# Kernel tuning notes

Measured on AMD Instinct MI355X. Metric: run time of the kernel, lower is better.

## Reference

```python
import jax, jax.numpy as jnp
import numpy as np

IMAGE_SIZE = 1024
DOWNSIZING = 64
THRESHOLD = 0.65  # default_threshold_target (threshold arg == 0)
NUM_BG_POINTS = 1
ORI_SHAPE = (2160, 3840)
EMBED_C, FEAT_H, FEAT_W = 256, 64, 64


def setup_inputs() -> dict:
    key = jax.random.key(0)
    k1, k2 = jax.random.split(key)
    image_embeddings = jax.random.normal(k1, (1, EMBED_C, FEAT_H, FEAT_W), dtype=jnp.float32)
    reference_feat = jax.random.normal(k2, (1, EMBED_C), dtype=jnp.float32) * 0.1
    ori_shape = jnp.array(ORI_SHAPE, dtype=jnp.int32)
    return {"image_embeddings": image_embeddings, "reference_feat": reference_feat, "ori_shape": ori_shape}


def _postprocess_masks(sim, H, W):
    # F.interpolate to (image_size, image_size), crop to pre-padded size, resize to ori_shape
    sim = jax.image.resize(sim, (1, 1, IMAGE_SIZE, IMAGE_SIZE), method="bilinear", antialias=False)
    scale = IMAGE_SIZE / max(H, W)
    ph = int(np.floor(H * scale + 0.5))
    pw = int(np.floor(W * scale + 0.5))
    sim = sim[..., :ph, :pw]
    return jax.image.resize(sim, (1, 1, H, W), method="bilinear", antialias=False)


def reference(image_embeddings, reference_feat, ori_shape):
    H, W = int(ori_shape[0]), int(ori_shape[1])
    # --- similarity map ---
    t = image_embeddings[0]                                   # (C, hf, wf)
    c, hf, wf = t.shape
    t = t / jnp.linalg.norm(t, axis=0, keepdims=True)         # channel-wise L2 norm
    sim = (reference_feat @ t.reshape(c, hf * wf)).reshape(1, 1, hf, wf)
    sim = _postprocess_masks(sim, H, W)
    m = sim[0, 0]                                             # (H, W)
    flat = m.reshape(-1)                                      # (H*W,)
    hw = H * W

    # --- background points: k smallest values ---
    _, bg_idx = jax.lax.top_k(-flat, NUM_BG_POINTS)
    bg_row = bg_idx // W
    bg_col = bg_idx % W
    bg_coords = jnp.stack([bg_col, bg_row], axis=1).astype(jnp.float32)  # (N, 2) = (x, y)

    # --- foreground points: grid-binned per-cell max (segment-max form of
    #     torch.where + unique + broadcast-equality + per-bin topk) ---
    ratio = IMAGE_SIZE / max(H, W)
    n_cells_side = IMAGE_SIZE // DOWNSIZING                    # 16; bounds grid rows/cols
    num_cells = n_cells_side * n_cells_side                    # 256 fixed
    idx = jnp.arange(hw, dtype=jnp.int32)
    ys = idx // W
    xs = idx % W
    gy = jnp.floor(ys * (ratio / DOWNSIZING)).astype(jnp.int32)
    gx = jnp.floor(xs * (ratio / DOWNSIZING)).astype(jnp.int32)
    seg = gy * n_cells_side + gx                               # grid id per pixel

    valid = flat > THRESHOLD
    masked = jnp.where(valid, flat, -jnp.inf)
    seg_max = jax.ops.segment_max(masked, seg, num_segments=num_cells)
    # first pixel achieving the cell max (matches torch.topk tie behavior)
    is_max = valid & (masked == seg_max[seg])
    cand = jnp.where(is_max, idx, hw)
    best = jax.ops.segment_min(cand, seg, num_segments=num_cells)
    cell_valid = best < hw
    bi = jnp.minimum(best, hw - 1)
    px = (bi % W).astype(jnp.float32)
    py = (bi // W).astype(jnp.float32)
    ps = flat[bi]
    points = jnp.stack([px, py, ps], axis=1)                   # (num_cells, 3) = (x, y, score)
    points = jnp.where(cell_valid[:, None], points, -1.0)      # mimic F.pad(value=-1) rows
    sort_key = jnp.where(cell_valid, ps, -jnp.inf)
    order = jnp.argsort(-sort_key)                             # score descending, invalid last
    points_scores = points[order]
    return points_scores, bg_coords
```

## Files before the change

### kernel.cpp

```cpp
#include <hip/hip_runtime.h>

#define W_OUT 3840
#define H_OUT 2160
#define IW 1024
#define IH 576

__device__ __forceinline__ unsigned int enc_f32(float f) {
    unsigned int b = __float_as_uint(f);
    return b ^ (0x80000000u | (unsigned int)((int)b >> 31));
}

__global__ __launch_bounds__(256) void sim_kernel(
    const float* __restrict__ emb, const float* __restrict__ ref,
    float* __restrict__ sim)
{
    const int lane = threadIdx.x & 63;
    const int wave = threadIdx.x >> 6;
    const int p = blockIdx.x * 64 + lane;
    const int cbase = wave * 64;
    float dot = 0.f, ss = 0.f;
#pragma unroll 8
    for (int cc = 0; cc < 64; ++cc) {
        int c = cbase + cc;
        float a = emb[c * 4096 + p];
        dot = fmaf(ref[c], a, dot);
        ss  = fmaf(a, a, ss);
    }
    __shared__ float sdot[4][64];
    __shared__ float sss[4][64];
    sdot[wave][lane] = dot;
    sss[wave][lane]  = ss;
    __syncthreads();
    if (wave == 0) {
        float d = (sdot[0][lane] + sdot[1][lane]) + (sdot[2][lane] + sdot[3][lane]);
        float s = (sss[0][lane] + sss[1][lane]) + (sss[2][lane] + sss[3][lane]);
        sim[p] = d / sqrtf(s);
    }
}

__global__ __launch_bounds__(256) void inter_kernel(
    const float* __restrict__ sim, float* __restrict__ I)
{
    const int a   = blockIdx.x;
    const int tid = threadIdx.x;
    const float INV16 = 0.0625f;

    float fa  = ((float)a + 0.5f) * INV16 - 0.5f;
    float faf = floorf(fa);
    float wa  = fa - faf;
    int si = (int)faf;
    int s1 = min(max(si + 1, 0), 63);
    int s0 = min(max(si,     0), 63);
    const float* row0 = sim + s0 * 64;
    const float* row1 = sim + s1 * 64;

    float4 o;
    float* po = &o.x;
#pragma unroll
    for (int k = 0; k < 4; ++k) {
        int b = tid * 4 + k;
        float fb  = ((float)b + 0.5f) * INV16 - 0.5f;
        float fbf = floorf(fb);
        float wb  = fb - fbf;
        int ci = (int)fbf;
        int c1 = min(max(ci + 1, 0), 63);
        int c0 = min(max(ci,     0), 63);
        float v0 = row0[c0] * (1.f - wb) + row0[c1] * wb;
        float v1 = row1[c0] * (1.f - wb) + row1[c1] * wb;
        po[k] = v0 * (1.f - wa) + v1 * wa;
    }
    *(float4*)(I + a * IW + tid * 4) = o;
}

__global__ __launch_bounds__(256) void scan_kernel(
    const float* __restrict__ I,
    unsigned long long* __restrict__ cellPart,
    unsigned long long* __restrict__ bgPart)
{
    const float INV375 = (float)(1.0 / 3.75);
    const int y   = blockIdx.x;
    const int tid = threadIdx.x;

    float fy  = ((float)y + 0.5f) * INV375 - 0.5f;
    float fyf = floorf(fy);
    float wy  = fy - fyf;
    int ai = (int)fyf;
    int a1 = min(max(ai + 1, 0), IH - 1);
    int a0 = min(max(ai,     0), IH - 1);
    const float* R0 = I + a0 * IW;
    const float* R1 = I + a1 * IW;

    unsigned long long bestCell = 0ull;
    unsigned long long bestBg   = 0xFFFFFFFFFFFFFFFFull;
    const int x0 = tid * 15;
    const unsigned int idxBase = (unsigned int)(y * W_OUT + x0);

#define UPD(F, jj) {                                                        \
        unsigned long long top = ((unsigned long long)enc_f32(F)) << 32;    \
        unsigned int idx = idxBase + (jj);                                  \
        unsigned long long bgk = top | (unsigned long long)idx;             \
        unsigned long long ck  = top | (unsigned long long)(~idx);          \
        if (ck  > bestCell) bestCell = ck;                                  \
        if (bgk < bestBg)   bestBg   = bgk;                                 \
    }

    if (tid == 0 || tid == 255) {
#pragma unroll
        for (int j = 0; j < 15; ++j) {
            int x = x0 + j;
            float fx  = ((float)x + 0.5f) * INV375 - 0.5f;
            float fxf = floorf(fx);
            float wx  = fx - fxf;
            int bi = (int)fxf;
            int b1 = min(max(bi + 1, 0), IW - 1);
            int b0 = min(max(bi,     0), IW - 1);
            float v0 = R0[b0] * (1.f - wx) + R0[b1] * wx;
            float v1 = R1[b0] * (1.f - wx) + R1[b1] * wx;
            float F  = v0 * (1.f - wy) + v1 * wy;
            UPD(F, j)
        }
    } else {
        const float* b0p = R0 + 4 * tid;
        const float* b1p = R1 + 4 * tid;
        float4 B0 = *(const float4*)b0p;
        float4 B1 = *(const float4*)b1p;
        const float f0[6] = {b0p[-1], B0.x, B0.y, B0.z, B0.w, b0p[4]};
        const float f1[6] = {b1p[-1], B1.x, B1.y, B1.z, B1.w, b1p[4]};

#define PX(j, i0) {                                                         \
            float fx  = ((float)(x0 + (j)) + 0.5f) * INV375 - 0.5f;         \
            float fxf = floorf(fx);                                         \
            float wx  = fx - fxf;                                           \
            float v0 = f0[(i0)] * (1.f - wx) + f0[(i0) + 1] * wx;           \
            float v1 = f1[(i0)] * (1.f - wx) + f1[(i0) + 1] * wx;           \
            float F  = v0 * (1.f - wy) + v1 * wy;                           \
            UPD(F, j)                                                       \
        }
        PX(0,0)  PX(1,0)  PX(2,1)  PX(3,1)  PX(4,1)
        PX(5,1)  PX(6,2)  PX(7,2)  PX(8,2)  PX(9,3)
        PX(10,3) PX(11,3) PX(12,3) PX(13,4) PX(14,4)
#undef PX
    }
#undef UPD

#pragma unroll
    for (int m = 1; m <= 8; m <<= 1) {
        unsigned long long o = __shfl_xor(bestCell, m, 64);
        if (o > bestCell) bestCell = o;
    }
    if ((tid & 15) == 0) cellPart[y * 16 + (tid >> 4)] = bestCell;

#pragma unroll
    for (int m = 1; m <= 32; m <<= 1) {
        unsigned long long o = __shfl_xor(bestBg, m, 64);
        if (o < bestBg) bestBg = o;
    }
    if ((tid & 63) == 0) bgPart[y * 4 + (tid >> 6)] = bestBg;
}

__global__ __launch_bounds__(256) void finalize_kernel(
    const unsigned long long* __restrict__ cellPart,
    const unsigned long long* __restrict__ bgPart,
    float* __restrict__ out)
{
    __shared__ unsigned long long sB[9 * 256];
    __shared__ float sk[256];
    __shared__ unsigned long long sb[256];
    const int t = threadIdx.x;

#pragma unroll
    for (int band = 0; band < 9; ++band) {
        unsigned long long acc = 0ull;
        const unsigned long long* p = cellPart + band * 3840 + t;
#pragma unroll
        for (int j = 0; j < 15; ++j) {
            unsigned long long k = p[j * 256];
            if (k > acc) acc = k;
        }
        sB[band * 256 + t] = acc;
    }

    unsigned long long m = 0xFFFFFFFFFFFFFFFFull;
    for (int i = t; i < H_OUT * 4; i += 256) {
        unsigned long long k = bgPart[i];
        if (k < m) m = k;
    }
    sb[t] = m;
    __syncthreads();

    unsigned long long best = 0ull;
    if (t < 144) {
        int band = t >> 4, cx = t & 15;
#pragma unroll
        for (int k = 0; k < 16; ++k) {
            unsigned long long v = sB[band * 256 + k * 16 + cx];
            if (v > best) best = v;
        }
    }
    float px = -1.f, py = -1.f, ps = -1.f;
    float key = -__builtin_huge_valf();
    if (best != 0ull) {
        unsigned int e = (unsigned int)(best >> 32);
        unsigned int b = (e & 0x80000000u) ? (e ^ 0x80000000u) : ~e;
        float v = __uint_as_float(b);
        if (v > 0.65f) {
            unsigned int idx = ~((unsigned int)(best & 0xFFFFFFFFull));
            px = (float)(idx % W_OUT);
            py = (float)(idx / W_OUT);
            ps = v;
            key = v;
        }
    }

    for (int s = 128; s > 0; s >>= 1) {
        if (t < s) {
            unsigned long long o = sb[t + s];
            if (o < sb[t]) sb[t] = o;
        }
        __syncthreads();
    }

    sk[t] = key;
    __syncthreads();
    int rank = 0;
    for (int j = 0; j < 256; ++j) {
        float kj = sk[j];
        if (kj > key || (kj == key && j < t)) rank++;
    }
    out[rank * 3 + 0] = px;
    out[rank * 3 + 1] = py;
    out[rank * 3 + 2] = ps;
    if (t == 0) {
        unsigned int idx = (unsigned int)(sb[0] & 0xFFFFFFFFull);
        out[256 * 3 + 0] = (float)(idx % W_OUT);
        out[256 * 3 + 1] = (float)(idx / W_OUT);
    }
}

extern "C" void kernel_launch(void* const* d_in, const int* in_sizes, int n_in,
                              void* d_out, int out_size, void* d_ws, size_t ws_size,
                              hipStream_t stream) {
    (void)in_sizes; (void)n_in; (void)out_size; (void)ws_size;
    const float* emb = (const float*)d_in[0];
    const float* ref = (const float*)d_in[1];
    float* out = (float*)d_out;

    float* sim = (float*)d_ws;
    float* I   = (float*)((char*)d_ws + 16384);
    unsigned long long* cellPart = (unsigned long long*)((char*)d_ws + 16384 + IH * IW * 4);
    unsigned long long* bgPart   = cellPart + H_OUT * 16;

    sim_kernel<<<64, 256, 0, stream>>>(emb, ref, sim);
    inter_kernel<<<IH, 256, 0, stream>>>(sim, I);
    scan_kernel<<<H_OUT, 256, 0, stream>>>(I, cellPart, bgPart);
    finalize_kernel<<<1, 256, 0, stream>>>(cellPart, bgPart, out);
}
```

Before: 100.8 us.

## Fuse sim into interpolation kernel and finalize into scan via last-block counter

Merges the four launches into two. Each interpolation block now recomputes the two similarity rows it needs from the embeddings, so the separate sim kernel is gone at the cost of redundant channel reads (each row is recomputed by about 16 blocks). The finalize work runs in whichever scan block increments an atomic counter last, behind a threadfence, which removes another launch. The counter is reset in the first kernel, so correctness depends on stream ordering between the two launches.

```diff
diff --git a/kernel.cpp b/kernel.cpp
--- a/kernel.cpp
+++ b/kernel.cpp
@@ -10,50 +10,55 @@
     return b ^ (0x80000000u | (unsigned int)((int)b >> 31));
 }
 
-__global__ __launch_bounds__(256) void sim_kernel(
+__global__ __launch_bounds__(256) void sim_inter_kernel(
     const float* __restrict__ emb, const float* __restrict__ ref,
-    float* __restrict__ sim)
+    float* __restrict__ I, unsigned int* __restrict__ counter)
 {
-    const int lane = threadIdx.x & 63;
-    const int wave = threadIdx.x >> 6;
-    const int p = blockIdx.x * 64 + lane;
-    const int cbase = wave * 64;
-    float dot = 0.f, ss = 0.f;
-#pragma unroll 8
-    for (int cc = 0; cc < 64; ++cc) {
-        int c = cbase + cc;
-        float a = emb[c * 4096 + p];
-        dot = fmaf(ref[c], a, dot);
-        ss  = fmaf(a, a, ss);
-    }
-    __shared__ float sdot[4][64];
-    __shared__ float sss[4][64];
-    sdot[wave][lane] = dot;
-    sss[wave][lane]  = ss;
-    __syncthreads();
-    if (wave == 0) {
-        float d = (sdot[0][lane] + sdot[1][lane]) + (sdot[2][lane] + sdot[3][lane]);
-        float s = (sss[0][lane] + sss[1][lane]) + (sss[2][lane] + sss[3][lane]);
-        sim[p] = d / sqrtf(s);
-    }
-}
-
-__global__ __launch_bounds__(256) void inter_kernel(
-    const float* __restrict__ sim, float* __restrict__ I)
-{
-    const int a   = blockIdx.x;
-    const int tid = threadIdx.x;
+    const int a    = blockIdx.x;
+    const int tid  = threadIdx.x;
+    const int lane = tid & 63;
+    const int wave = tid >> 6;
+
+    if (a == 0 && tid == 0) *counter = 0;
+
     const float INV16 = 0.0625f;
-
     float fa  = ((float)a + 0.5f) * INV16 - 0.5f;
     float faf = floorf(fa);
     float wa  = fa - faf;
     int si = (int)faf;
     int s1 = min(max(si + 1, 0), 63);
     int s0 = min(max(si,     0), 63);
-    const float* row0 = sim + s0 * 64;
-    const float* row1 = sim + s1 * 64;
-
+
+    __shared__ float sdot[4][64];
+    __shared__ float sss[4][64];
+    __shared__ float simR[2][64];
+
+    const int rows[2] = {s0, s1};
+#pragma unroll
+    for (int r = 0; r < 2; ++r) {
+        const int p = rows[r] * 64 + lane;
+        const int cbase = wave * 64;
+        float dot = 0.f, ss = 0.f;
+#pragma unroll 8
+        for (int cc = 0; cc < 64; ++cc) {
+            int c = cbase + cc;
+            float v = emb[c * 4096 + p];
+            dot = fmaf(ref[c], v, dot);
+            ss  = fmaf(v, v, ss);
+        }
+        sdot[wave][lane] = dot;
+        sss[wave][lane]  = ss;
+        __syncthreads();
+        if (wave == 0) {
+            float d = (sdot[0][lane] + sdot[1][lane]) + (sdot[2][lane] + sdot[3][lane]);
+            float s = (sss[0][lane] + sss[1][lane]) + (sss[2][lane] + sss[3][lane]);
+            simR[r][lane] = d / sqrtf(s);
+        }
+        __syncthreads();
+    }
+
+    const float* row0 = simR[0];
+    const float* row1 = simR[1];
     float4 o;
     float* po = &o.x;
 #pragma unroll
@@ -72,11 +77,18 @@
     *(float4*)(I + a * IW + tid * 4) = o;
 }
 
-__global__ __launch_bounds__(256) void scan_kernel(
+__global__ __launch_bounds__(256) void scan_finalize_kernel(
     const float* __restrict__ I,
     unsigned long long* __restrict__ cellPart,
-    unsigned long long* __restrict__ bgPart)
+    unsigned long long* __restrict__ bgPart,
+    unsigned int* __restrict__ counter,
+    float* __restrict__ out)
 {
+    __shared__ unsigned long long sB[9 * 256];
+    __shared__ float sk[256];
+    __shared__ unsigned long long sb[256];
+    __shared__ unsigned int isLast;
+
     const float INV375 = (float)(1.0 / 3.75);
     const int y   = blockIdx.x;
     const int tid = threadIdx.x;
@@ -156,41 +168,37 @@
         if (o < bestBg) bestBg = o;
     }
     if ((tid & 63) == 0) bgPart[y * 4 + (tid >> 6)] = bestBg;
-}
-
-__global__ __launch_bounds__(256) void finalize_kernel(
-    const unsigned long long* __restrict__ cellPart,
-    const unsigned long long* __restrict__ bgPart,
-    float* __restrict__ out)
-{
-    __shared__ unsigned long long sB[9 * 256];
-    __shared__ float sk[256];
-    __shared__ unsigned long long sb[256];
-    const int t = threadIdx.x;
+
+    __threadfence();
+    __syncthreads();
+    if (tid == 0) isLast = (atomicAdd(counter, 1u) == (unsigned)(H_OUT - 1)) ? 1u : 0u;
+    __syncthreads();
+    if (!isLast) return;
+    __threadfence();
 
 #pragma unroll
     for (int band = 0; band < 9; ++band) {
         unsigned long long acc = 0ull;
-        const unsigned long long* p = cellPart + band * 3840 + t;
+        const unsigned long long* p = cellPart + band * 3840 + tid;
 #pragma unroll
         for (int j = 0; j < 15; ++j) {
             unsigned long long k = p[j * 256];
             if (k > acc) acc = k;
         }
-        sB[band * 256 + t] = acc;
+        sB[band * 256 + tid] = acc;
     }
 
     unsigned long long m = 0xFFFFFFFFFFFFFFFFull;
-    for (int i = t; i < H_OUT * 4; i += 256) {
+    for (int i = tid; i < H_OUT * 4; i += 256) {
         unsigned long long k = bgPart[i];
         if (k < m) m = k;
     }
-    sb[t] = m;
+    sb[tid] = m;
     __syncthreads();
 
     unsigned long long best = 0ull;
-    if (t < 144) {
-        int band = t >> 4, cx = t & 15;
+    if (tid < 144) {
+        int band = tid >> 4, cx = tid & 15;
 #pragma unroll
         for (int k = 0; k < 16; ++k) {
             unsigned long long v = sB[band * 256 + k * 16 + cx];
@@ -213,24 +221,24 @@
     }
 
     for (int s = 128; s > 0; s >>= 1) {
-        if (t < s) {
-            unsigned long long o = sb[t + s];
-            if (o < sb[t]) sb[t] = o;
+        if (tid < s) {
+            unsigned long long o = sb[tid + s];
+            if (o < sb[tid]) sb[tid] = o;
         }
         __syncthreads();
     }
 
-    sk[t] = key;
+    sk[tid] = key;
     __syncthreads();
     int rank = 0;
     for (int j = 0; j < 256; ++j) {
         float kj = sk[j];
-        if (kj > key || (kj == key && j < t)) rank++;
+        if (kj > key || (kj == key && j < tid)) rank++;
     }
     out[rank * 3 + 0] = px;
     out[rank * 3 + 1] = py;
     out[rank * 3 + 2] = ps;
-    if (t == 0) {
+    if (tid == 0) {
         unsigned int idx = (unsigned int)(sb[0] & 0xFFFFFFFFull);
         out[256 * 3 + 0] = (float)(idx % W_OUT);
         out[256 * 3 + 1] = (float)(idx / W_OUT);
@@ -245,13 +253,11 @@
     const float* ref = (const float*)d_in[1];
     float* out = (float*)d_out;
 
-    float* sim = (float*)d_ws;
-    float* I   = (float*)((char*)d_ws + 16384);
-    unsigned long long* cellPart = (unsigned long long*)((char*)d_ws + 16384 + IH * IW * 4);
+    float* I = (float*)d_ws;
+    unsigned long long* cellPart = (unsigned long long*)((char*)d_ws + IH * IW * 4);
     unsigned long long* bgPart   = cellPart + H_OUT * 16;
-
-    sim_kernel<<<64, 256, 0, stream>>>(emb, ref, sim);
-    inter_kernel<<<IH, 256, 0, stream>>>(sim, I);
-    scan_kernel<<<H_OUT, 256, 0, stream>>>(I, cellPart, bgPart);
-    finalize_kernel<<<1, 256, 0, stream>>>(cellPart, bgPart, out);
-}
+    unsigned int* counter        = (unsigned int*)(bgPart + H_OUT * 4);
+
+    sim_inter_kernel<<<IH, 256, 0, stream>>>(emb, ref, I, counter);
+    scan_finalize_kernel<<<H_OUT, 256, 0, stream>>>(I, cellPart, bgPart, counter, out);
+}
```

Result: slower. 243.2 us (+141.3%).
